# Kernel optimization log

Hardware: AMD Instinct MI355X
Metric: run time of the kernel (lower is better)

The kernel has to match this reference:

```python
import jax, jax.numpy as jnp
import numpy as np

D_IN, D_MAIN, D_BLOCK = 32, 128, 256
LN_EPS = 1e-5


def _ln(x, g, b):
    mu = x.mean(-1, keepdims=True)
    var = ((x - mu) ** 2).mean(-1, keepdims=True)
    return (x - mu) / jnp.sqrt(var + LN_EPS) * g + b


def setup_inputs() -> dict:
    key = jax.random.key(0)
    ks = iter(jax.random.split(key, 64))
    nrm = lambda shape, s=0.05: jax.random.normal(next(ks), shape, dtype=jnp.float32) * s
    inp = {
        'x_num': jax.random.normal(next(ks), (256, D_IN), dtype=jnp.float32),
        'candidate_x_num': jax.random.normal(next(ks), (100000, D_IN), dtype=jnp.float32),
        'candidate_y': jax.random.normal(next(ks), (100000,), dtype=jnp.float32),
        'context_size': 96,
        # input linear
        'lin_W': nrm((D_IN, D_MAIN), 0.15), 'lin_b': nrm((D_MAIN,)),
        # encoder block 0 (no prenorm)
        'e0_W1': nrm((D_MAIN, D_BLOCK)), 'e0_b1': nrm((D_BLOCK,)),
        'e0_W2': nrm((D_BLOCK, D_MAIN)), 'e0_b2': nrm((D_MAIN,)),
        # encoder block 1 (prenorm)
        'e1_g': jnp.ones((D_MAIN,), jnp.float32), 'e1_b': jnp.zeros((D_MAIN,), jnp.float32),
        'e1_W1': nrm((D_MAIN, D_BLOCK)), 'e1_b1': nrm((D_BLOCK,)),
        'e1_W2': nrm((D_BLOCK, D_MAIN)), 'e1_b2': nrm((D_MAIN,)),
        # mixer normalization + K projection
        'mix_g': jnp.ones((D_MAIN,), jnp.float32), 'mix_b': jnp.zeros((D_MAIN,), jnp.float32),
        'K_W': nrm((D_MAIN, D_MAIN)), 'K_b': nrm((D_MAIN,)),
        # T module (Linear -> ReLU -> Linear(no bias))
        'T_W1': nrm((D_MAIN, D_BLOCK)), 'T_b1': nrm((D_BLOCK,)),
        'T_W2': nrm((D_BLOCK, D_MAIN)),
        'lab_w': nrm((D_MAIN,), 0.5), 'lab_b': nrm((D_MAIN,), 0.5),
        # predictor block (prenorm)
        'p0_g': jnp.ones((D_MAIN,), jnp.float32), 'p0_b': jnp.zeros((D_MAIN,), jnp.float32),
        'p0_W1': nrm((D_MAIN, D_BLOCK)), 'p0_b1': nrm((D_BLOCK,)),
        'p0_W2': nrm((D_BLOCK, D_MAIN)), 'p0_b2': nrm((D_MAIN,)),
        # head
        'head_g': jnp.ones((D_MAIN,), jnp.float32), 'head_b': jnp.zeros((D_MAIN,), jnp.float32),
        'head_W': nrm((D_MAIN, 1)), 'head_bias': nrm((1,)),
    }
    return inp


def _encode(xn, lin_W, lin_b, e0_W1, e0_b1, e0_W2, e0_b2,
            e1_g, e1_b, e1_W1, e1_b1, e1_W2, e1_b2,
            mix_g, mix_b, K_W, K_b):
    h = xn @ lin_W + lin_b
    # block 0: Linear -> ReLU -> Linear, residual (dropout=0)
    h = h + jax.nn.relu(h @ e0_W1 + e0_b1) @ e0_W2 + e0_b2
    # block 1: prenorm
    h = h + jax.nn.relu(_ln(h, e1_g, e1_b) @ e1_W1 + e1_b1) @ e1_W2 + e1_b2
    k = _ln(h, mix_g, mix_b) @ K_W + K_b
    return h, k


def reference(x_num, candidate_x_num, candidate_y, context_size,
              lin_W, lin_b, e0_W1, e0_b1, e0_W2, e0_b2,
              e1_g, e1_b, e1_W1, e1_b1, e1_W2, e1_b2,
              mix_g, mix_b, K_W, K_b, T_W1, T_b1, T_W2,
              lab_w, lab_b, p0_g, p0_b, p0_W1, p0_b1, p0_W2, p0_b2,
              head_g, head_b, head_W, head_bias):
    enc = lambda xn: _encode(xn, lin_W, lin_b, e0_W1, e0_b1, e0_W2, e0_b2,
                             e1_g, e1_b, e1_W1, e1_b1, e1_W2, e1_b2,
                             mix_g, mix_b, K_W, K_b)
    candidate_k = enc(candidate_x_num)[1]            # [N, d]
    x, k = enc(x_num)                                # [B, d] each
    # squared L2 distances [B, N] without materializing [B, N, d]
    d2 = (jnp.sum(k * k, -1, keepdims=True)
          - 2.0 * (k @ candidate_k.T)
          + jnp.sum(candidate_k * candidate_k, -1)[None, :])
    _, context_idx = jax.lax.top_k(-d2, context_size)  # k smallest -> [B, K]
    context_k = candidate_k[context_idx]               # [B, K, d]
    # similarities = -||k - context_k||^2 (same expansion as torch code)
    sims = (-jnp.sum(k * k, -1, keepdims=True)
            + 2.0 * jnp.einsum('bd,bkd->bk', k, context_k)
            - jnp.sum(context_k * context_k, -1))
    probs = jax.nn.softmax(sims, axis=-1)              # [B, K]
    context_y_emb = candidate_y[context_idx][..., None] * lab_w + lab_b  # [B, K, d]
    t = jax.nn.relu((k[:, None, :] - context_k) @ T_W1 + T_b1) @ T_W2    # [B, K, d]
    values = context_y_emb + t
    context_x = jnp.einsum('bk,bkd->bd', probs, values)
    x = x + context_x
    # predictor block (prenorm)
    x = x + jax.nn.relu(_ln(x, p0_g, p0_b) @ p0_W1 + p0_b1) @ p0_W2 + p0_b2
    # head: LN -> ReLU -> Linear
    out = jax.nn.relu(_ln(x, head_g, head_b)) @ head_W + head_bias
    return out
```

## Files before the change

kernel.cpp:

```cpp
#include <hip/hip_runtime.h>
#include <hip/hip_fp16.h>
#include <float.h>
#include <math.h>

#define D_IN 32
#define D_MAIN 128
#define D_BLOCK 256
#define CTX 96
#define LN_EPS 1e-5f

typedef _Float16 f16x8 __attribute__((ext_vector_type(8)));
typedef float f32x4 __attribute__((ext_vector_type(4)));
typedef unsigned short ushort4v __attribute__((ext_vector_type(4)));

__device__ __forceinline__ unsigned short f2h(float x) {
  return __half_as_ushort(__float2half(x));
}
__device__ __forceinline__ float h2f(unsigned short u) {
  return __half2float(__ushort_as_half(u));
}

struct PackJobs {
  const float* W[8];
  unsigned short* out[8];
  int K[8];
  int N[8];
  int cum[9];
};

__global__ __launch_bounds__(256) void prep_kernel(
    PackJobs pj, int* __restrict__ ghist, int na, int* __restrict__ scount, int nb)
{
  const int tid = blockIdx.x * 256 + threadIdx.x;
  if (tid < na) ghist[tid] = 0;
  else if (tid - na < nb) scount[tid - na] = 0;
  if (tid >= pj.cum[8]) return;
  int j = 0;
#pragma unroll
  for (int i = 1; i < 8; ++i)
    if (tid >= pj.cum[i]) j = i;
  const int lt = tid - pj.cum[j];
  const int K = pj.K[j], N = pj.N[j];
  const float* __restrict__ W = pj.W[j];
  const int l = lt & 63, f = lt >> 6;
  const int ks = K / 32;
  const int s = f % ks, jb = f / ks;
  const int kb = s * 32 + (l >> 4) * 8;
  const int n = jb * 16 + (l & 15);
  unsigned short v[8];
#pragma unroll
  for (int e = 0; e < 8; ++e) v[e] = f2h(W[(size_t)(kb + e) * N + n]);
  ushort4v* o = (ushort4v*)(pj.out[j] + (size_t)lt * 8);
  ushort4v u0 = {v[0], v[1], v[2], v[3]};
  ushort4v u1 = {v[4], v[5], v[6], v[7]};
  o[0] = u0; o[1] = u1;
}

#define LDA 136
#define LDU 72

__device__ __forceinline__ void mlp_block(
    f32x4 (&h)[4][4], unsigned short* __restrict__ As, unsigned short* __restrict__ Us,
    const unsigned short* __restrict__ W1_pk, const float* __restrict__ b1,
    const unsigned short* __restrict__ W2_pk, const float* __restrict__ b2,
    int mrow, int nw, int c, int q, int lane)
{
#pragma unroll 1
  for (int ch = 0; ch < 4; ++ch) {
    f16x8 b1f[4][2];
#pragma unroll
    for (int s = 0; s < 4; ++s)
#pragma unroll
      for (int ntl = 0; ntl < 2; ++ntl) {
        const int j = ch*4 + nw*2 + ntl;
        b1f[s][ntl] = *(const f16x8*)&W1_pk[((size_t)(j*4 + s) * 64 + lane) * 8];
      }
    f32x4 u[4][2];
#pragma unroll
    for (int mi = 0; mi < 4; ++mi)
#pragma unroll
      for (int ntl = 0; ntl < 2; ++ntl) { f32x4 z = {0.f,0.f,0.f,0.f}; u[mi][ntl] = z; }
#pragma unroll
    for (int s = 0; s < 4; ++s) {
      f16x8 a[4];
#pragma unroll
      for (int mi = 0; mi < 4; ++mi)
        a[mi] = *(const f16x8*)&As[(mrow + mi*16 + c) * LDA + s*32 + q*8];
#pragma unroll
      for (int ntl = 0; ntl < 2; ++ntl)
#pragma unroll
        for (int mi = 0; mi < 4; ++mi)
          u[mi][ntl] = __builtin_amdgcn_mfma_f32_16x16x32_f16(a[mi], b1f[s][ntl], u[mi][ntl], 0, 0, 0);
    }
    f16x8 b2f[2][4];
#pragma unroll
    for (int s2 = 0; s2 < 2; ++s2)
#pragma unroll
      for (int nt = 0; nt < 4; ++nt) {
        const int j2 = nw*4 + nt;
        b2f[s2][nt] = *(const f16x8*)&W2_pk[((size_t)(j2*8 + ch*2 + s2) * 64 + lane) * 8];
      }
#pragma unroll
    for (int ntl = 0; ntl < 2; ++ntl) {
      const int colg = ch*64 + nw*32 + ntl*16 + c;
      const float bb = b1[colg];
      const int coll = nw*32 + ntl*16 + c;
#pragma unroll
      for (int mi = 0; mi < 4; ++mi)
#pragma unroll
        for (int r = 0; r < 4; ++r)
          Us[(mrow + mi*16 + q*4 + r) * LDU + coll] = f2h(fmaxf(u[mi][ntl][r] + bb, 0.f));
    }
    __syncthreads();
#pragma unroll
    for (int s2 = 0; s2 < 2; ++s2) {
      f16x8 a2[4];
#pragma unroll
      for (int mi = 0; mi < 4; ++mi)
        a2[mi] = *(const f16x8*)&Us[(mrow + mi*16 + c) * LDU + s2*32 + q*8];
#pragma unroll
      for (int nt = 0; nt < 4; ++nt)
#pragma unroll
        for (int mi = 0; mi < 4; ++mi)
          h[mi][nt] = __builtin_amdgcn_mfma_f32_16x16x32_f16(a2[mi], b2f[s2][nt], h[mi][nt], 0, 0, 0);
    }
    __syncthreads();
  }
  if (b2) {
#pragma unroll
    for (int nt = 0; nt < 4; ++nt) {
      const float bb = b2[nw*64 + nt*16 + c];
#pragma unroll
      for (int mi = 0; mi < 4; ++mi) {
        h[mi][nt][0] += bb; h[mi][nt][1] += bb; h[mi][nt][2] += bb; h[mi][nt][3] += bb;
      }
    }
  }
}

#define LDA2 136
#define LDU2 264

struct Enc64Shared {
  unsigned short As[64 * LDA2];
  unsigned short Us[64 * LDU2];
};

__device__ __forceinline__ void mlp64(
    f32x4 (&h)[4][2], unsigned short* __restrict__ As, unsigned short* __restrict__ Us,
    const unsigned short* __restrict__ W1_pk, const float* __restrict__ b1,
    const unsigned short* __restrict__ W2_pk, const float* __restrict__ b2,
    int w, int c, int q, int lane)
{
  f16x8 b1f[4][4];
#pragma unroll
  for (int s = 0; s < 4; ++s)
#pragma unroll
    for (int ntl = 0; ntl < 4; ++ntl) {
      const int j = w*4 + ntl;
      b1f[s][ntl] = *(const f16x8*)&W1_pk[((size_t)(j*4 + s) * 64 + lane) * 8];
    }
  f32x4 u[4][4];
#pragma unroll
  for (int mi = 0; mi < 4; ++mi)
#pragma unroll
    for (int ntl = 0; ntl < 4; ++ntl) { f32x4 z = {0.f,0.f,0.f,0.f}; u[mi][ntl] = z; }
#pragma unroll
  for (int s = 0; s < 4; ++s) {
    f16x8 a[4];
#pragma unroll
    for (int mi = 0; mi < 4; ++mi)
      a[mi] = *(const f16x8*)&As[(mi*16 + c) * LDA2 + s*32 + q*8];
#pragma unroll
    for (int ntl = 0; ntl < 4; ++ntl)
#pragma unroll
      for (int mi = 0; mi < 4; ++mi)
        u[mi][ntl] = __builtin_amdgcn_mfma_f32_16x16x32_f16(a[mi], b1f[s][ntl], u[mi][ntl], 0, 0, 0);
  }
  f16x8 b2f[8][2];
#pragma unroll
  for (int s2 = 0; s2 < 8; ++s2)
#pragma unroll
    for (int nt = 0; nt < 2; ++nt) {
      const int j2 = w*2 + nt;
      b2f[s2][nt] = *(const f16x8*)&W2_pk[((size_t)(j2*8 + s2) * 64 + lane) * 8];
    }
#pragma unroll
  for (int ntl = 0; ntl < 4; ++ntl) {
    const int colg = w*64 + ntl*16 + c;
    const float bb = b1[colg];
#pragma unroll
    for (int mi = 0; mi < 4; ++mi)
#pragma unroll
      for (int r = 0; r < 4; ++r)
        Us[(mi*16 + q*4 + r) * LDU2 + colg] = f2h(fmaxf(u[mi][ntl][r] + bb, 0.f));
  }
  __syncthreads();
#pragma unroll
  for (int s2 = 0; s2 < 8; ++s2) {
    f16x8 a2[4];
#pragma unroll
    for (int mi = 0; mi < 4; ++mi)
      a2[mi] = *(const f16x8*)&Us[(mi*16 + c) * LDU2 + s2*32 + q*8];
#pragma unroll
    for (int nt = 0; nt < 2; ++nt)
#pragma unroll
      for (int mi = 0; mi < 4; ++mi)
        h[mi][nt] = __builtin_amdgcn_mfma_f32_16x16x32_f16(a2[mi], b2f[s2][nt], h[mi][nt], 0, 0, 0);
  }
  __syncthreads();
  if (b2) {
#pragma unroll
    for (int nt = 0; nt < 2; ++nt) {
      const float bb = b2[w*32 + nt*16 + c];
#pragma unroll
      for (int mi = 0; mi < 4; ++mi) {
        h[mi][nt][0] += bb; h[mi][nt][1] += bb; h[mi][nt][2] += bb; h[mi][nt][3] += bb;
      }
    }
  }
}

__device__ __forceinline__ void ln64(
    f32x4 (&h)[4][2], unsigned short* __restrict__ As, float* __restrict__ sc,
    const float* __restrict__ g, const float* __restrict__ bv,
    int w, int c, int q)
{
  float* lsum = sc;
  float* lssq = sc + 256;
  float ps[4][4], pss[4][4];
#pragma unroll
  for (int mi = 0; mi < 4; ++mi)
#pragma unroll
    for (int r = 0; r < 4; ++r) {
      float s = 0.f, ss = 0.f;
#pragma unroll
      for (int nt = 0; nt < 2; ++nt) { const float v = h[mi][nt][r]; s += v; ss += v * v; }
      ps[mi][r] = s; pss[mi][r] = ss;
    }
#pragma unroll
  for (int off = 1; off < 16; off <<= 1) {
#pragma unroll
    for (int mi = 0; mi < 4; ++mi)
#pragma unroll
      for (int r = 0; r < 4; ++r) {
        ps[mi][r] += __shfl_xor(ps[mi][r], off, 64);
        pss[mi][r] += __shfl_xor(pss[mi][r], off, 64);
      }
  }
#pragma unroll
  for (int r = 0; r < 4; ++r) {
    if (c == r) {
#pragma unroll
      for (int mi = 0; mi < 4; ++mi) {
        const int row = mi*16 + q*4 + r;
        lsum[w*64 + row] = ps[mi][r];
        lssq[w*64 + row] = pss[mi][r];
      }
    }
  }
  float gg[2], bb[2];
#pragma unroll
  for (int nt = 0; nt < 2; ++nt) {
    const int col = w*32 + nt*16 + c;
    gg[nt] = g[col]; bb[nt] = bv[col];
  }
  __syncthreads();
#pragma unroll
  for (int mi = 0; mi < 4; ++mi)
#pragma unroll
    for (int r = 0; r < 4; ++r) {
      const int row = mi*16 + q*4 + r;
      const float s  = lsum[row] + lsum[64 + row] + lsum[128 + row] + lsum[192 + row];
      const float ss = lssq[row] + lssq[64 + row] + lssq[128 + row] + lssq[192 + row];
      const float mu = s * (1.f / 128.f);
      const float rs = rsqrtf(ss * (1.f / 128.f) - mu * mu + LN_EPS);
#pragma unroll
      for (int nt = 0; nt < 2; ++nt) {
        const int col = w*32 + nt*16 + c;
        As[row * LDA2 + col] = f2h((h[mi][nt][r] - mu) * rs * gg[nt] + bb[nt]);
      }
    }
  __syncthreads();
}

__global__ __launch_bounds__(256, 2) void encode64(
    const float* __restrict__ cand_x, int N, int encC,
    const float* __restrict__ x_num, int B,
    const unsigned short* __restrict__ linW_pk, const float* __restrict__ lin_b,
    const unsigned short* __restrict__ e0W1_pk, const float* __restrict__ e0_b1,
    const unsigned short* __restrict__ e0W2_pk, const float* __restrict__ e0_b2,
    const float* __restrict__ e1_g, const float* __restrict__ e1_b,
    const unsigned short* __restrict__ e1W1_pk, const float* __restrict__ e1_b1,
    const unsigned short* __restrict__ e1W2_pk, const float* __restrict__ e1_b2,
    const float* __restrict__ mix_g, const float* __restrict__ mix_b,
    const unsigned short* __restrict__ KW_pk, const float* __restrict__ K_b,
    unsigned short* __restrict__ ckb, float* __restrict__ ckf,
    float* __restrict__ cknorm,
    float* __restrict__ xk, float* __restrict__ xh)
{
  __shared__ Enc64Shared sh;
  float* sc = (float*)sh.Us;
  const int t = threadIdx.x, lane = t & 63, w = t >> 6;
  const int c = lane & 15, q = lane >> 4;
  const bool isCand = (int)blockIdx.x < encC;
  const float* __restrict__ src = isCand ? cand_x : x_num;
  const int nrows = isCand ? N : B;
  const int row0 = (isCand ? (int)blockIdx.x : ((int)blockIdx.x - encC)) * 64;

  for (int i = t; i < 64 * 8; i += 256) {
    const int r = i >> 3, c4 = (i & 7) * 4;
    const int gr = row0 + r;
    float4 v = make_float4(0.f, 0.f, 0.f, 0.f);
    if (gr < nrows) v = *(const float4*)&src[(size_t)gr * D_IN + c4];
    ushort4v u = {f2h(v.x), f2h(v.y), f2h(v.z), f2h(v.w)};
    *(ushort4v*)&sh.As[r * LDA2 + c4] = u;
  }
  __syncthreads();

  f32x4 h[4][2];
  {
    f16x8 bl[2];
#pragma unroll
    for (int nt = 0; nt < 2; ++nt)
      bl[nt] = *(const f16x8*)&linW_pk[((size_t)(w*2 + nt) * 64 + lane) * 8];
    f16x8 a[4];
#pragma unroll
    for (int mi = 0; mi < 4; ++mi)
      a[mi] = *(const f16x8*)&sh.As[(mi*16 + c) * LDA2 + q*8];
#pragma unroll
    for (int nt = 0; nt < 2; ++nt) {
      const float bb = lin_b[(w*2 + nt)*16 + c];
#pragma unroll
      for (int mi = 0; mi < 4; ++mi) {
        f32x4 z = {0.f, 0.f, 0.f, 0.f};
        z = __builtin_amdgcn_mfma_f32_16x16x32_f16(a[mi], bl[nt], z, 0, 0, 0);
        z[0] += bb; z[1] += bb; z[2] += bb; z[3] += bb;
        h[mi][nt] = z;
      }
    }
  }
  __syncthreads();
#pragma unroll
  for (int nt = 0; nt < 2; ++nt)
#pragma unroll
    for (int mi = 0; mi < 4; ++mi)
#pragma unroll
      for (int r = 0; r < 4; ++r)
        sh.As[(mi*16 + q*4 + r) * LDA2 + w*32 + nt*16 + c] = f2h(h[mi][nt][r]);
  __syncthreads();

  mlp64(h, sh.As, sh.Us, e0W1_pk, e0_b1, e0W2_pk, e0_b2, w, c, q, lane);
  ln64(h, sh.As, sc, e1_g, e1_b, w, c, q);
  mlp64(h, sh.As, sh.Us, e1W1_pk, e1_b1, e1W2_pk, e1_b2, w, c, q, lane);
  ln64(h, sh.As, sc, mix_g, mix_b, w, c, q);

  if (!isCand) {
#pragma unroll
    for (int nt = 0; nt < 2; ++nt) {
      const int col = w*32 + nt*16 + c;
#pragma unroll
      for (int mi = 0; mi < 4; ++mi)
#pragma unroll
        for (int r = 0; r < 4; ++r) {
          const int gr = row0 + mi*16 + q*4 + r;
          if (gr < nrows) xh[(size_t)gr * D_MAIN + col] = h[mi][nt][r];
        }
    }
  }

  f16x8 bk[4][2];
#pragma unroll
  for (int s = 0; s < 4; ++s)
#pragma unroll
    for (int nt = 0; nt < 2; ++nt) {
      const int j = w*2 + nt;
      bk[s][nt] = *(const f16x8*)&KW_pk[((size_t)(j*4 + s) * 64 + lane) * 8];
    }
  f32x4 kk[4][2];
#pragma unroll
  for (int mi = 0; mi < 4; ++mi)
#pragma unroll
    for (int nt = 0; nt < 2; ++nt) { f32x4 z = {0.f,0.f,0.f,0.f}; kk[mi][nt] = z; }
#pragma unroll
  for (int s = 0; s < 4; ++s) {
    f16x8 a[4];
#pragma unroll
    for (int mi = 0; mi < 4; ++mi)
      a[mi] = *(const f16x8*)&sh.As[(mi*16 + c) * LDA2 + s*32 + q*8];
#pragma unroll
    for (int nt = 0; nt < 2; ++nt)
#pragma unroll
      for (int mi = 0; mi < 4; ++mi)
        kk[mi][nt] = __builtin_amdgcn_mfma_f32_16x16x32_f16(a[mi], bk[s][nt], kk[mi][nt], 0, 0, 0);
  }

  if (isCand) {
#pragma unroll
    for (int nt = 0; nt < 2; ++nt) {
      const int col = w*32 + nt*16 + c;
      const float bb = K_b[col];
#pragma unroll
      for (int mi = 0; mi < 4; ++mi)
#pragma unroll
        for (int r = 0; r < 4; ++r) {
          const float v = kk[mi][nt][r] + bb;
          kk[mi][nt][r] = v;
          const int gr = row0 + mi*16 + q*4 + r;
          if (gr < nrows) {
            if (ckf) ckf[(size_t)gr * D_MAIN + col] = v;
            ckb[(size_t)gr * D_MAIN + col] = f2h(v);
          }
        }
    }
    float pss[4][4];
#pragma unroll
    for (int mi = 0; mi < 4; ++mi)
#pragma unroll
      for (int r = 0; r < 4; ++r) {
        float ss = 0.f;
#pragma unroll
        for (int nt = 0; nt < 2; ++nt) { const float v = kk[mi][nt][r]; ss += v * v; }
        pss[mi][r] = ss;
      }
#pragma unroll
    for (int off = 1; off < 16; off <<= 1)
#pragma unroll
      for (int mi = 0; mi < 4; ++mi)
#pragma unroll
        for (int r = 0; r < 4; ++r)
          pss[mi][r] += __shfl_xor(pss[mi][r], off, 64);
#pragma unroll
    for (int r = 0; r < 4; ++r) {
      if (c == r) {
#pragma unroll
        for (int mi = 0; mi < 4; ++mi)
          sc[w*64 + mi*16 + q*4 + r] = pss[mi][r];
      }
    }
    __syncthreads();
    if (t < 64) {
      const int gr = row0 + t;
      if (gr < nrows) cknorm[gr] = sc[t] + sc[64 + t] + sc[128 + t] + sc[192 + t];
    }
  } else {
#pragma unroll
    for (int nt = 0; nt < 2; ++nt) {
      const int col = w*32 + nt*16 + c;
      const float bb = K_b[col];
#pragma unroll
      for (int mi = 0; mi < 4; ++mi)
#pragma unroll
        for (int r = 0; r < 4; ++r) {
          const int gr = row0 + mi*16 + q*4 + r;
          if (gr < nrows) xk[(size_t)gr * D_MAIN + col] = kk[mi][nt][r] + bb;
        }
    }
  }
}

__global__ __launch_bounds__(256) void score_mfma(
    const float* __restrict__ xk, const unsigned short* __restrict__ ckb,
    const float* __restrict__ cknorm, int N, int Npad,
    __half* __restrict__ S)
{
  __shared__ unsigned short Ks[64 * 136];
  const int t = threadIdx.x, lane = t & 63, w = t >> 6;
  const int c = lane & 15, q = lane >> 4;
  const int b0 = blockIdx.y * 64;
  const int n0 = blockIdx.x * 256 + w * 64;

  f16x8 bf[4][4];
#pragma unroll
  for (int s = 0; s < 4; ++s)
#pragma unroll
    for (int nt = 0; nt < 4; ++nt) {
      const size_t n = (size_t)(n0 + nt*16 + c);
      bf[s][nt] = *(const f16x8*)&ckb[n * D_MAIN + s*32 + q*8];
    }

  for (int i = t; i < 64 * 32; i += 256) {
    const int r = i >> 5, c4 = (i & 31) * 4;
    const float4 v = *(const float4*)&xk[(size_t)(b0 + r) * D_MAIN + c4];
    ushort4v u = {f2h(v.x), f2h(v.y), f2h(v.z), f2h(v.w)};
    *(ushort4v*)&Ks[r * 136 + c4] = u;
  }
  __syncthreads();

  f32x4 acc[4][4];
#pragma unroll
  for (int mi = 0; mi < 4; ++mi)
#pragma unroll
    for (int nt = 0; nt < 4; ++nt) { f32x4 z = {0.f,0.f,0.f,0.f}; acc[mi][nt] = z; }

#pragma unroll
  for (int s = 0; s < 4; ++s) {
    f16x8 a[4];
#pragma unroll
    for (int mi = 0; mi < 4; ++mi)
      a[mi] = *(const f16x8*)&Ks[(mi*16 + c) * 136 + s*32 + q*8];
#pragma unroll
    for (int nt = 0; nt < 4; ++nt)
#pragma unroll
      for (int mi = 0; mi < 4; ++mi)
        acc[mi][nt] = __builtin_amdgcn_mfma_f32_16x16x32_f16(a[mi], bf[s][nt], acc[mi][nt], 0, 0, 0);
  }
#pragma unroll
  for (int nt = 0; nt < 4; ++nt) {
    const int col = n0 + nt*16 + c;
    const float cn = (col < N) ? cknorm[col] : 0.f;
#pragma unroll
    for (int mi = 0; mi < 4; ++mi)
#pragma unroll
      for (int r = 0; r < 4; ++r) {
        const int row = b0 + mi*16 + q*4 + r;
        const float sv = (col < N) ? (2.f * acc[mi][nt][r] - cn) : -65504.f;
        S[(size_t)row * Npad + col] = __float2half(sv);
      }
  }
}

#define TK_CHUNK 12800
#define TK_RBINS 4096
#define TK_SCAP 2048

__device__ __forceinline__ unsigned flip2(unsigned u) {
  const unsigned m = (u >> 15) & 0x00010001u;
  const unsigned xm = (m * 0xFFFFu) | ((m ^ 0x00010001u) * 0x8000u);
  return u ^ xm;
}

__global__ __launch_bounds__(256) void thist_kernel(
    const __half* __restrict__ S, int Npad, int* __restrict__ ghist)
{
  __shared__ int lh[TK_RBINS];
  const int t = threadIdx.x;
  const int row = blockIdx.y;
  const int c0 = blockIdx.x * TK_CHUNK;
  const int jend = min(c0 + TK_CHUNK, Npad);
  for (int i = t; i < TK_RBINS; i += 256) lh[i] = 0;
  __syncthreads();
  const unsigned* rp = (const unsigned*)(S + (size_t)row * Npad);
  for (int j = c0 + t * 8; j < jend; j += 2048) {
    const uint4 v = *(const uint4*)(rp + (j >> 1));
    const unsigned k0 = flip2(v.x), k1 = flip2(v.y);
    const unsigned k2 = flip2(v.z), k3 = flip2(v.w);
    atomicAdd(&lh[(k0 & 0xFFFFu) >> 4], 1); atomicAdd(&lh[k0 >> 20], 1);
    atomicAdd(&lh[(k1 & 0xFFFFu) >> 4], 1); atomicAdd(&lh[k1 >> 20], 1);
    atomicAdd(&lh[(k2 & 0xFFFFu) >> 4], 1); atomicAdd(&lh[k2 >> 20], 1);
    atomicAdd(&lh[(k3 & 0xFFFFu) >> 4], 1); atomicAdd(&lh[k3 >> 20], 1);
  }
  __syncthreads();
  int* gh = ghist + (size_t)row * TK_RBINS;
  for (int i = t; i < TK_RBINS; i += 256) {
    const int v = lh[i];
    if (v) atomicAdd(&gh[i], v);
  }
}

__global__ __launch_bounds__(256) void tthresh_kernel(
    const int* __restrict__ ghist, int* __restrict__ thr)
{
  __shared__ int sp[257];
  const int t = threadIdx.x;
  const int row = blockIdx.x;
  const int* gh = ghist + (size_t)row * TK_RBINS;
  int s = 0;
#pragma unroll
  for (int i = 0; i < 16; ++i) s += gh[t * 16 + i];
  sp[t] = s;
  if (t == 0) sp[256] = 0;
  __syncthreads();
  for (int off = 1; off < 256; off <<= 1) {
    const int v = (t + off < 256) ? sp[t + off] : 0;
    __syncthreads();
    sp[t] += v;
    __syncthreads();
  }
  if (sp[t] >= CTX && (t == 255 || sp[t + 1] < CTX)) {
    int running = (t == 255) ? 0 : sp[t + 1];
    int T = t * 16;
    for (int b = t * 16 + 15; b >= t * 16; --b) {
      running += gh[b];
      if (running >= CTX) { T = b; break; }
    }
    thr[row] = T;
  }
}

__global__ __launch_bounds__(256) void tcollect_kernel(
    const __half* __restrict__ S, int Npad, const int* __restrict__ thr,
    int* __restrict__ scount, unsigned long long* __restrict__ surv)
{
  const int t = threadIdx.x;
  const int row = blockIdx.y;
  const int c0 = blockIdx.x * TK_CHUNK;
  const int jend = min(c0 + TK_CHUNK, Npad);
  const int T = thr[row];
  const unsigned* rp = (const unsigned*)(S + (size_t)row * Npad);
  unsigned long long* sv = surv + (size_t)row * TK_SCAP;
  for (int j = c0 + t * 8; j < jend; j += 2048) {
    const uint4 v = *(const uint4*)(rp + (j >> 1));
    unsigned ks[4] = {flip2(v.x), flip2(v.y), flip2(v.z), flip2(v.w)};
#pragma unroll
    for (int wqi = 0; wqi < 4; ++wqi) {
      const unsigned klo = ks[wqi] & 0xFFFFu;
      const unsigned khi = ks[wqi] >> 16;
      const int jlo = j + wqi * 2, jhi = j + wqi * 2 + 1;
      if ((int)(klo >> 4) >= T) {
        const int pos = atomicAdd(&scount[row], 1);
        if (pos < TK_SCAP)
          sv[pos] = ((unsigned long long)klo << 32) | (0xFFFFFFFFu - (unsigned)jlo);
      }
      if ((int)(khi >> 4) >= T) {
        const int pos = atomicAdd(&scount[row], 1);
        if (pos < TK_SCAP)
          sv[pos] = ((unsigned long long)khi << 32) | (0xFFFFFFFFu - (unsigned)jhi);
      }
    }
  }
}

__global__ __launch_bounds__(1024) void tsort_kernel(
    const unsigned long long* __restrict__ surv, const int* __restrict__ scount,
    int* __restrict__ idx_out)
{
  __shared__ unsigned long long sb[TK_SCAP];
  const int t = threadIdx.x;
  const int row = blockIdx.x;
  const int m = min(scount[row], TK_SCAP);
  int P = 128;
  while (P < m) P <<= 1;
  const unsigned long long* sv = surv + (size_t)row * TK_SCAP;
  for (int i = t; i < P; i += 1024)
    sb[i] = (i < m) ? sv[i] : 0x00000000FFFFFFFFull;
  __syncthreads();
  for (int k = 2; k <= P; k <<= 1) {
    for (int j = k >> 1; j > 0; j >>= 1) {
      for (int i = t; i < P; i += 1024) {
        const int ixj = i ^ j;
        if (ixj > i) {
          const unsigned long long a = sb[i], b = sb[ixj];
          const bool desc = ((i & k) == 0);
          if ((a < b) == desc) { sb[i] = b; sb[ixj] = a; }
        }
      }
      __syncthreads();
    }
  }
  if (t < CTX)
    idx_out[row * CTX + t] = (int)(0xFFFFFFFFu - (unsigned)(sb[t] & 0xFFFFFFFFu));
}

struct TmodShared {
  unsigned short As[128 * LDA];
  unsigned short Us[128 * LDU];
  float part[2][128];
  float probs[128];
  float sims[128];
  float kb[128];
  float xhs[128];
  float ys[128];
  int   idxs[128];
  float ubuf[256];
  float vbuf[256];
  float xr[128];
  float dl[128];
  float scal[4];
};

__global__ __launch_bounds__(256, 2) void tmod_kernel(
    const float* __restrict__ xh, const float* __restrict__ xk,
    const unsigned short* __restrict__ ckb, const float* __restrict__ ckf,
    const float* __restrict__ cand_y, const int* __restrict__ ctx_idx,
    const unsigned short* __restrict__ TW1_pk, const float* __restrict__ T_b1,
    const unsigned short* __restrict__ TW2_pk,
    const float* __restrict__ lab_w, const float* __restrict__ lab_b,
    const float* __restrict__ p0_g, const float* __restrict__ p0_b,
    const float* __restrict__ p0_W1, const float* __restrict__ p0_b1,
    const float* __restrict__ p0_W2, const float* __restrict__ p0_b2,
    const float* __restrict__ head_g, const float* __restrict__ head_b,
    const float* __restrict__ head_W, const float* __restrict__ head_bias,
    float* __restrict__ out)
{
  __shared__ TmodShared sh;
  const int t = threadIdx.x, lane = t & 63, w = t >> 6;
  const int mw = w & 1, nw = w >> 1;
  const int c = lane & 15, q = lane >> 4;
  const int mrow = mw * 64;
  const int b = blockIdx.x;
  float* spart = (float*)sh.Us;

  if (t < 128) {
    sh.ys[t] = 0.f;
    if (t < CTX) {
      const int j = ctx_idx[b * CTX + t];
      sh.idxs[t] = j;
      sh.ys[t] = cand_y[j];
    }
  }
  if (t < 32) {
    *(float4*)&sh.kb[t * 4] = *(const float4*)&xk[(size_t)b * D_MAIN + t * 4];
  } else if (t < 64) {
    const int i = t - 32;
    *(float4*)&sh.xhs[i * 4] = *(const float4*)&xh[(size_t)b * D_MAIN + i * 4];
  }
  __syncthreads();

  for (int i = t; i < 128 * 16; i += 256) {
    const int r = i >> 4, seg = i & 15, c0 = seg * 8;
    if (r < CTX) {
      float v0x, v0y, v0z, v0w, v1x, v1y, v1z, v1w;
      if (ckf) {
        const float* cr = &ckf[(size_t)sh.idxs[r] * D_MAIN + c0];
        const float4 v0 = *(const float4*)cr;
        const float4 v1 = *(const float4*)(cr + 4);
        v0x = v0.x; v0y = v0.y; v0z = v0.z; v0w = v0.w;
        v1x = v1.x; v1y = v1.y; v1z = v1.z; v1w = v1.w;
      } else {
        const unsigned short* cr = &ckb[(size_t)sh.idxs[r] * D_MAIN + c0];
        const ushort4v u0 = *(const ushort4v*)cr;
        const ushort4v u1 = *(const ushort4v*)(cr + 4);
        v0x = h2f(u0[0]); v0y = h2f(u0[1]); v0z = h2f(u0[2]); v0w = h2f(u0[3]);
        v1x = h2f(u1[0]); v1y = h2f(u1[1]); v1z = h2f(u1[2]); v1w = h2f(u1[3]);
      }
      const float4 k0 = *(const float4*)&sh.kb[c0];
      const float4 k1 = *(const float4*)&sh.kb[c0 + 4];
      const float d0 = k0.x - v0x, d1 = k0.y - v0y, d2 = k0.z - v0z, d3 = k0.w - v0w;
      const float d4 = k1.x - v1x, d5 = k1.y - v1y, d6 = k1.z - v1z, d7 = k1.w - v1w;
      ushort4v u0s = {f2h(d0), f2h(d1), f2h(d2), f2h(d3)};
      ushort4v u1s = {f2h(d4), f2h(d5), f2h(d6), f2h(d7)};
      *(ushort4v*)&sh.As[r * LDA + c0] = u0s;
      *(ushort4v*)&sh.As[r * LDA + c0 + 4] = u1s;
      spart[r * 16 + seg] = d0*d0 + d1*d1 + d2*d2 + d3*d3 + d4*d4 + d5*d5 + d6*d6 + d7*d7;
    } else {
      ushort4v z = {0, 0, 0, 0};
      *(ushort4v*)&sh.As[r * LDA + c0] = z;
      *(ushort4v*)&sh.As[r * LDA + c0 + 4] = z;
    }
  }
  __syncthreads();
  if (t < 128) {
    float s = 0.f;
    if (t < CTX) {
#pragma unroll
      for (int seg = 0; seg < 16; ++seg) s += spart[t * 16 + seg];
      sh.sims[t] = -s;
    } else {
      sh.sims[t] = -FLT_MAX;
    }
  }
  __syncthreads();
  if (t < 64) {
    float m = fmaxf(sh.sims[t], sh.sims[t + 64]);
#pragma unroll
    for (int off = 32; off > 0; off >>= 1) m = fmaxf(m, __shfl_xor(m, off, 64));
    if (t == 0) sh.scal[0] = m;
  }
  __syncthreads();
  if (t < 128) {
    const float e = (t < CTX) ? __expf(sh.sims[t] - sh.scal[0]) : 0.f;
    sh.probs[t] = e;
  }
  __syncthreads();
  if (t < 64) {
    float s = sh.probs[t] + sh.probs[t + 64];
#pragma unroll
    for (int off = 32; off > 0; off >>= 1) s += __shfl_xor(s, off, 64);
    if (t == 0) sh.scal[1] = 1.f / s;
  }
  __syncthreads();
  if (t < 128) sh.probs[t] *= sh.scal[1];
  __syncthreads();
  if (t < 64) {
    float sy = sh.probs[t] * sh.ys[t] + sh.probs[t + 64] * sh.ys[t + 64];
#pragma unroll
    for (int off = 32; off > 0; off >>= 1) sy += __shfl_xor(sy, off, 64);
    if (t == 0) sh.scal[2] = sy;
  }
  __syncthreads();

  f32x4 h[4][4];
#pragma unroll
  for (int mi = 0; mi < 4; ++mi)
#pragma unroll
    for (int nt = 0; nt < 4; ++nt) { f32x4 z = {0.f,0.f,0.f,0.f}; h[mi][nt] = z; }
  mlp_block(h, sh.As, sh.Us, TW1_pk, T_b1, TW2_pk, nullptr, mrow, nw, c, q, lane);

#pragma unroll
  for (int nt = 0; nt < 4; ++nt) {
    float p = 0.f;
#pragma unroll
    for (int mi = 0; mi < 4; ++mi)
#pragma unroll
      for (int r = 0; r < 4; ++r)
        p += sh.probs[mrow + mi*16 + q*4 + r] * h[mi][nt][r];
    p += __shfl_xor(p, 16, 64);
    p += __shfl_xor(p, 32, 64);
    if (q == 0) sh.part[mw][nw*64 + nt*16 + c] = p;
  }
  __syncthreads();

  if (t < 128)
    sh.xr[t] = sh.xhs[t] + sh.part[0][t] + sh.part[1][t] + sh.scal[2] * lab_w[t] + lab_b[t];
  __syncthreads();
  if (t < 64) {
    float s = sh.xr[t] + sh.xr[t + 64];
    float ss = sh.xr[t]*sh.xr[t] + sh.xr[t+64]*sh.xr[t+64];
#pragma unroll
    for (int off = 32; off > 0; off >>= 1) {
      s += __shfl_xor(s, off, 64);
      ss += __shfl_xor(ss, off, 64);
    }
    if (t == 0) {
      const float mu = s * (1.f / 128.f);
      sh.scal[0] = mu;
      sh.scal[1] = rsqrtf(ss * (1.f / 128.f) - mu * mu + LN_EPS);
    }
  }
  __syncthreads();
  if (t < 128)
    sh.dl[t] = (sh.xr[t] - sh.scal[0]) * sh.scal[1] * p0_g[t] + p0_b[t];
  __syncthreads();
  {
    float u = 0.f;
    for (int cc = 0; cc < D_MAIN; cc += 4) {
      const float w0 = p0_W1[(cc + 0) * D_BLOCK + t];
      const float w1 = p0_W1[(cc + 1) * D_BLOCK + t];
      const float w2 = p0_W1[(cc + 2) * D_BLOCK + t];
      const float w3 = p0_W1[(cc + 3) * D_BLOCK + t];
      const float4 d4 = *(const float4*)&sh.dl[cc];
      u += d4.x * w0 + d4.y * w1 + d4.z * w2 + d4.w * w3;
    }
    sh.ubuf[t] = fmaxf(u + p0_b1[t], 0.f);
  }
  __syncthreads();
  {
    const int cc = t & 127;
    const int d0 = (t >> 7) * 128;
    float v = 0.f;
    for (int d = d0; d < d0 + 128; d += 4) {
      const float w0 = p0_W2[(d + 0) * D_MAIN + cc];
      const float w1 = p0_W2[(d + 1) * D_MAIN + cc];
      const float w2 = p0_W2[(d + 2) * D_MAIN + cc];
      const float w3 = p0_W2[(d + 3) * D_MAIN + cc];
      const float4 u4 = *(const float4*)&sh.ubuf[d];
      v += u4.x * w0 + u4.y * w1 + u4.z * w2 + u4.w * w3;
    }
    sh.vbuf[t] = v;
  }
  __syncthreads();
  if (t < 128) sh.xr[t] += sh.vbuf[t] + sh.vbuf[t + 128] + p0_b2[t];
  __syncthreads();
  if (t < 64) {
    float s = sh.xr[t] + sh.xr[t + 64];
    float ss = sh.xr[t]*sh.xr[t] + sh.xr[t+64]*sh.xr[t+64];
#pragma unroll
    for (int off = 32; off > 0; off >>= 1) {
      s += __shfl_xor(s, off, 64);
      ss += __shfl_xor(ss, off, 64);
    }
    if (t == 0) {
      const float mu = s * (1.f / 128.f);
      sh.scal[0] = mu;
      sh.scal[1] = rsqrtf(ss * (1.f / 128.f) - mu * mu + LN_EPS);
    }
  }
  __syncthreads();
  if (t < 128) {
    float hv = (sh.xr[t] - sh.scal[0]) * sh.scal[1] * head_g[t] + head_b[t];
    sh.dl[t] = fmaxf(hv, 0.f) * head_W[t];
  }
  __syncthreads();
  if (t < 64) {
    float s = sh.dl[t] + sh.dl[t + 64];
#pragma unroll
    for (int off = 32; off > 0; off >>= 1) s += __shfl_xor(s, off, 64);
    if (t == 0) out[b] = s + head_bias[0];
  }
}

extern "C" void kernel_launch(void* const* d_in, const int* in_sizes, int n_in,
                              void* d_out, int out_size, void* d_ws, size_t ws_size,
                              hipStream_t stream)
{
  const float* x_num   = (const float*)d_in[0];
  const float* cand_x  = (const float*)d_in[1];
  const float* cand_y  = (const float*)d_in[2];
  const float* lin_W   = (const float*)d_in[4];
  const float* lin_b   = (const float*)d_in[5];
  const float* e0_W1   = (const float*)d_in[6];
  const float* e0_b1   = (const float*)d_in[7];
  const float* e0_W2   = (const float*)d_in[8];
  const float* e0_b2   = (const float*)d_in[9];
  const float* e1_g    = (const float*)d_in[10];
  const float* e1_b    = (const float*)d_in[11];
  const float* e1_W1   = (const float*)d_in[12];
  const float* e1_b1   = (const float*)d_in[13];
  const float* e1_W2   = (const float*)d_in[14];
  const float* e1_b2   = (const float*)d_in[15];
  const float* mix_g   = (const float*)d_in[16];
  const float* mix_b   = (const float*)d_in[17];
  const float* K_W     = (const float*)d_in[18];
  const float* K_b     = (const float*)d_in[19];
  const float* T_W1    = (const float*)d_in[20];
  const float* T_b1    = (const float*)d_in[21];
  const float* T_W2    = (const float*)d_in[22];
  const float* lab_w   = (const float*)d_in[23];
  const float* lab_b   = (const float*)d_in[24];
  const float* p0_g    = (const float*)d_in[25];
  const float* p0_b    = (const float*)d_in[26];
  const float* p0_W1   = (const float*)d_in[27];
  const float* p0_b1   = (const float*)d_in[28];
  const float* p0_W2   = (const float*)d_in[29];
  const float* p0_b2   = (const float*)d_in[30];
  const float* head_g  = (const float*)d_in[31];
  const float* head_b  = (const float*)d_in[32];
  const float* head_W  = (const float*)d_in[33];
  const float* head_bias = (const float*)d_in[34];
  float* out = (float*)d_out;

  const int N = in_sizes[1] / D_IN;
  const int B = in_sizes[0] / D_IN;
  const int Npad = ((N + 255) / 256) * 256;
  const int chunks = (Npad + TK_CHUNK - 1) / TK_CHUNK;

  char* p = (char*)d_ws;
  auto take = [&](size_t bytes) {
    char* q = p;
    p += (bytes + 255) & ~(size_t)255;
    return q;
  };
  unsigned short* pk_lin  = (unsigned short*)take(32  * 128 * 2);
  unsigned short* pk_e0w1 = (unsigned short*)take(128 * 256 * 2);
  unsigned short* pk_e0w2 = (unsigned short*)take(256 * 128 * 2);
  unsigned short* pk_e1w1 = (unsigned short*)take(128 * 256 * 2);
  unsigned short* pk_e1w2 = (unsigned short*)take(256 * 128 * 2);
  unsigned short* pk_kw   = (unsigned short*)take(128 * 128 * 2);
  unsigned short* pk_tw1  = (unsigned short*)take(128 * 256 * 2);
  unsigned short* pk_tw2  = (unsigned short*)take(256 * 128 * 2);
  unsigned short* ckb = (unsigned short*)take((size_t)Npad * D_MAIN * 2);
  float*  cknorm  = (float*)take((size_t)N * sizeof(float));
  float*  xh      = (float*)take((size_t)B * D_MAIN * sizeof(float));
  float*  xk      = (float*)take((size_t)B * D_MAIN * sizeof(float));
  __half* S       = (__half*)take((size_t)B * Npad * sizeof(__half));
  int*    ctxidx  = (int*)take((size_t)B * CTX * sizeof(int));
  int*    ghist   = (int*)take((size_t)B * TK_RBINS * sizeof(int));
  int*    thr     = (int*)take((size_t)B * sizeof(int));
  int*    scount  = (int*)take((size_t)B * sizeof(int));
  unsigned long long* surv =
      (unsigned long long*)take((size_t)B * TK_SCAP * sizeof(unsigned long long));
  float* ckf = nullptr;
  {
    const size_t used = (size_t)(p - (char*)d_ws);
    const size_t need = (size_t)Npad * D_MAIN * sizeof(float);
    if (used + need + 256 <= ws_size) ckf = (float*)take(need);
  }
  (void)n_in; (void)out_size;

  PackJobs pj;
  const float* ws_[8] = {lin_W, e0_W1, e0_W2, e1_W1, e1_W2, K_W, T_W1, T_W2};
  unsigned short* os_[8] = {pk_lin, pk_e0w1, pk_e0w2, pk_e1w1, pk_e1w2, pk_kw, pk_tw1, pk_tw2};
  const int Ks_[8] = {32, 128, 256, 128, 256, 128, 128, 256};
  const int Ns_[8] = {128, 256, 128, 256, 128, 128, 256, 128};
  pj.cum[0] = 0;
  for (int i = 0; i < 8; ++i) {
    pj.W[i] = ws_[i]; pj.out[i] = os_[i]; pj.K[i] = Ks_[i]; pj.N[i] = Ns_[i];
    pj.cum[i + 1] = pj.cum[i] + (Ns_[i] / 16) * (Ks_[i] / 32) * 64;
  }
  {
    const int na = B * TK_RBINS;
    const int total = (na + B > pj.cum[8]) ? (na + B) : pj.cum[8];
    prep_kernel<<<(total + 255) / 256, 256, 0, stream>>>(pj, ghist, na, scount, B);
  }

  const int encC = (N + 63) / 64;
  const int encB = (B + 63) / 64;
  encode64<<<encC + encB, 256, 0, stream>>>(
      cand_x, N, encC, x_num, B,
      pk_lin, lin_b, pk_e0w1, e0_b1, pk_e0w2, e0_b2,
      e1_g, e1_b, pk_e1w1, e1_b1, pk_e1w2, e1_b2,
      mix_g, mix_b, pk_kw, K_b,
      ckb, ckf, cknorm, xk, xh);

  dim3 sg(Npad / 256, B / 64);
  score_mfma<<<sg, 256, 0, stream>>>(xk, ckb, cknorm, N, Npad, S);

  dim3 tg(chunks, B);
  thist_kernel<<<tg, 256, 0, stream>>>(S, Npad, ghist);
  tthresh_kernel<<<B, 256, 0, stream>>>(ghist, thr);
  tcollect_kernel<<<tg, 256, 0, stream>>>(S, Npad, thr, scount, surv);
  tsort_kernel<<<B, 1024, 0, stream>>>(surv, scount, ctxidx);

  tmod_kernel<<<B, 256, 0, stream>>>(
      xh, xk, ckb, ckf, cand_y, ctxidx,
      pk_tw1, T_b1, pk_tw2, lab_w, lab_b,
      p0_g, p0_b, p0_W1, p0_b1, p0_W2, p0_b2,
      head_g, head_b, head_W, head_bias, out);
}
```

Measured before the change: 342.2 us.

## Stage score tile through LDS for coalesced stores; fuse threshold into collect

The score kernel now writes its fp16 output tile into shared memory and then stores full 16-byte rows to global memory, instead of scattered 2-byte stores from the MFMA fragment layout. Separately, the threshold-finding kernel is merged into the collect kernel: each collect block recomputes the histogram prefix scan for its row, which removes one launch and the thr buffer. The cost is extra LDS use and barriers in the score kernel, plus redundant scan work repeated across every chunk block.

```diff
diff --git a/kernel.cpp b/kernel.cpp
--- a/kernel.cpp
+++ b/kernel.cpp
@@ -12,6 +12,7 @@
 typedef _Float16 f16x8 __attribute__((ext_vector_type(8)));
 typedef float f32x4 __attribute__((ext_vector_type(4)));
 typedef unsigned short ushort4v __attribute__((ext_vector_type(4)));
+typedef unsigned short ushort8v __attribute__((ext_vector_type(8)));
 
 __device__ __forceinline__ unsigned short f2h(float x) {
   return __half_as_ushort(__float2half(x));
@@ -464,11 +465,15 @@
     const float* __restrict__ cknorm, int N, int Npad,
     __half* __restrict__ S)
 {
-  __shared__ unsigned short Ks[64 * 136];
+  __shared__ union {
+    unsigned short Ks[64 * 136];
+    unsigned short St[64 * 264];
+  } sh;
   const int t = threadIdx.x, lane = t & 63, w = t >> 6;
   const int c = lane & 15, q = lane >> 4;
   const int b0 = blockIdx.y * 64;
-  const int n0 = blockIdx.x * 256 + w * 64;
+  const int nblk = blockIdx.x * 256;
+  const int n0 = nblk + w * 64;
 
   f16x8 bf[4][4];
 #pragma unroll
@@ -483,7 +488,7 @@
     const int r = i >> 5, c4 = (i & 31) * 4;
     const float4 v = *(const float4*)&xk[(size_t)(b0 + r) * D_MAIN + c4];
     ushort4v u = {f2h(v.x), f2h(v.y), f2h(v.z), f2h(v.w)};
-    *(ushort4v*)&Ks[r * 136 + c4] = u;
+    *(ushort4v*)&sh.Ks[r * 136 + c4] = u;
   }
   __syncthreads();
 
@@ -498,25 +503,35 @@
     f16x8 a[4];
 #pragma unroll
     for (int mi = 0; mi < 4; ++mi)
-      a[mi] = *(const f16x8*)&Ks[(mi*16 + c) * 136 + s*32 + q*8];
+      a[mi] = *(const f16x8*)&sh.Ks[(mi*16 + c) * 136 + s*32 + q*8];
 #pragma unroll
     for (int nt = 0; nt < 4; ++nt)
 #pragma unroll
       for (int mi = 0; mi < 4; ++mi)
         acc[mi][nt] = __builtin_amdgcn_mfma_f32_16x16x32_f16(a[mi], bf[s][nt], acc[mi][nt], 0, 0, 0);
   }
+  __syncthreads();
+
 #pragma unroll
   for (int nt = 0; nt < 4; ++nt) {
-    const int col = n0 + nt*16 + c;
+    const int colin = w*64 + nt*16 + c;
+    const int col = nblk + colin;
     const float cn = (col < N) ? cknorm[col] : 0.f;
 #pragma unroll
     for (int mi = 0; mi < 4; ++mi)
 #pragma unroll
       for (int r = 0; r < 4; ++r) {
-        const int row = b0 + mi*16 + q*4 + r;
         const float sv = (col < N) ? (2.f * acc[mi][nt][r] - cn) : -65504.f;
-        S[(size_t)row * Npad + col] = __float2half(sv);
-      }
+        sh.St[(mi*16 + q*4 + r) * 264 + colin] = f2h(sv);
+      }
+  }
+  __syncthreads();
+  {
+    const int row = t >> 2, cb = (t & 3) * 64;
+    ushort8v* dst = (ushort8v*)(S + (size_t)(b0 + row) * Npad + nblk + cb);
+#pragma unroll
+    for (int i = 0; i < 8; ++i)
+      dst[i] = *(const ushort8v*)&sh.St[row * 264 + cb + i*8];
   }
 }
 
@@ -558,45 +573,42 @@
   }
 }
 
-__global__ __launch_bounds__(256) void tthresh_kernel(
-    const int* __restrict__ ghist, int* __restrict__ thr)
+__global__ __launch_bounds__(256) void tcollect_kernel(
+    const __half* __restrict__ S, int Npad, const int* __restrict__ ghist,
+    int* __restrict__ scount, unsigned long long* __restrict__ surv)
 {
   __shared__ int sp[257];
-  const int t = threadIdx.x;
-  const int row = blockIdx.x;
-  const int* gh = ghist + (size_t)row * TK_RBINS;
-  int s = 0;
-#pragma unroll
-  for (int i = 0; i < 16; ++i) s += gh[t * 16 + i];
-  sp[t] = s;
-  if (t == 0) sp[256] = 0;
-  __syncthreads();
-  for (int off = 1; off < 256; off <<= 1) {
-    const int v = (t + off < 256) ? sp[t + off] : 0;
-    __syncthreads();
-    sp[t] += v;
-    __syncthreads();
-  }
-  if (sp[t] >= CTX && (t == 255 || sp[t + 1] < CTX)) {
-    int running = (t == 255) ? 0 : sp[t + 1];
-    int T = t * 16;
-    for (int b = t * 16 + 15; b >= t * 16; --b) {
-      running += gh[b];
-      if (running >= CTX) { T = b; break; }
-    }
-    thr[row] = T;
-  }
-}
-
-__global__ __launch_bounds__(256) void tcollect_kernel(
-    const __half* __restrict__ S, int Npad, const int* __restrict__ thr,
-    int* __restrict__ scount, unsigned long long* __restrict__ surv)
-{
+  __shared__ int thrS;
   const int t = threadIdx.x;
   const int row = blockIdx.y;
+  const int* gh = ghist + (size_t)row * TK_RBINS;
+  {
+    int s = 0;
+#pragma unroll
+    for (int i = 0; i < 16; ++i) s += gh[t * 16 + i];
+    sp[t] = s;
+    if (t == 0) sp[256] = 0;
+    __syncthreads();
+    for (int off = 1; off < 256; off <<= 1) {
+      const int v = (t + off < 256) ? sp[t + off] : 0;
+      __syncthreads();
+      sp[t] += v;
+      __syncthreads();
+    }
+    if (sp[t] >= CTX && (t == 255 || sp[t + 1] < CTX)) {
+      int running = (t == 255) ? 0 : sp[t + 1];
+      int T = t * 16;
+      for (int b = t * 16 + 15; b >= t * 16; --b) {
+        running += gh[b];
+        if (running >= CTX) { T = b; break; }
+      }
+      thrS = T;
+    }
+    __syncthreads();
+  }
+  const int T = thrS;
   const int c0 = blockIdx.x * TK_CHUNK;
   const int jend = min(c0 + TK_CHUNK, Npad);
-  const int T = thr[row];
   const unsigned* rp = (const unsigned*)(S + (size_t)row * Npad);
   unsigned long long* sv = surv + (size_t)row * TK_SCAP;
   for (int j = c0 + t * 8; j < jend; j += 2048) {
@@ -946,7 +958,6 @@
   __half* S       = (__half*)take((size_t)B * Npad * sizeof(__half));
   int*    ctxidx  = (int*)take((size_t)B * CTX * sizeof(int));
   int*    ghist   = (int*)take((size_t)B * TK_RBINS * sizeof(int));
-  int*    thr     = (int*)take((size_t)B * sizeof(int));
   int*    scount  = (int*)take((size_t)B * sizeof(int));
   unsigned long long* surv =
       (unsigned long long*)take((size_t)B * TK_SCAP * sizeof(unsigned long long));
@@ -988,8 +999,7 @@
 
   dim3 tg(chunks, B);
   thist_kernel<<<tg, 256, 0, stream>>>(S, Npad, ghist);
-  tthresh_kernel<<<B, 256, 0, stream>>>(ghist, thr);
-  tcollect_kernel<<<tg, 256, 0, stream>>>(S, Npad, thr, scount, surv);
+  tcollect_kernel<<<tg, 256, 0, stream>>>(S, Npad, ghist, scount, surv);
   tsort_kernel<<<B, 1024, 0, stream>>>(surv, scount, ctxidx);
 
   tmod_kernel<<<B, 256, 0, stream>>>(
```

Measured after the change: 353.3 us. +3.2%, slower.
